# Performance work log

Hardware: AMD Instinct MI355X
Metric: run time of the kernel (lower is better)

Reference implementation:

```python
import jax, jax.numpy as jnp
import numpy as np

DEPTH = 3
DIM = 64
N_NODES = 4096
BATCH = 4


def setup_inputs() -> dict:
    key = jax.random.key(0)
    k1, k2, k3, k4 = jax.random.split(key, 4)
    x = jax.random.normal(k1, (BATCH, N_NODES, DIM), dtype=jnp.float32)
    graph = jax.random.uniform(k2, (BATCH, N_NODES, N_NODES), dtype=jnp.float32)
    # Linear((depth+1)*dim, dim): PyTorch default init U(-1/sqrt(fan_in), 1/sqrt(fan_in))
    fan_in = (DEPTH + 1) * DIM
    bound = 1.0 / np.sqrt(fan_in)
    W = jax.random.uniform(k3, (DIM, fan_in), minval=-bound, maxval=bound, dtype=jnp.float32)
    b = jax.random.uniform(k4, (DIM,), minval=-bound, maxval=bound, dtype=jnp.float32)
    return {"x": x, "graph": graph, "W": W, "b": b}


def reference(x, graph, W, b):
    # GCN branch of LocalGNN.forward (dropout p=0 -> identity).
    n = graph.shape[-1]
    g = graph + jnp.eye(n, dtype=graph.dtype)          # add self loops
    d = 1.0 / (jnp.sqrt(g.sum(axis=-1)) + 1e-7)        # [b, n]
    # D @ g @ D with D = diag(d):  g_ij * d_i * d_j
    g = g * d[..., :, None] * d[..., None, :]
    outs = [x]
    h = x
    for _ in range(DEPTH):
        h = jnp.einsum('bij,bjd->bid', g, h)           # dense propagation
        outs.append(h)
    cat = jnp.concatenate(outs, axis=-1)               # [b, n, (depth+1)*dim]
    return cat @ W.T + b
```

## Files before the change

kernel.cpp:

```cpp
#include <hip/hip_runtime.h>
#include <hip/hip_bf16.h>


typedef __attribute__((ext_vector_type(4))) float  floatx4;
typedef __attribute__((ext_vector_type(8))) short  short8;

#define NB 4
#define NN 4096
#define ND 64
#define HF_B 262144

__device__ __forceinline__ unsigned short f2bf_bits(float v) {
    __hip_bfloat16 b = __float2bfloat16(v);
    return *reinterpret_cast<unsigned short*>(&b);
}
__device__ __forceinline__ float bf2f(unsigned short u) {
    unsigned int x = ((unsigned int)u) << 16;
    return *reinterpret_cast<float*>(&x);
}
__device__ __forceinline__ short8 pack8p(const float* v) {
    short8 r;
#pragma unroll
    for (int j = 0; j < 8; ++j) r[j] = (short)f2bf_bits(v[j]);
    return r;
}

__global__ __launch_bounds__(256, 4) void prep_graph(const float* __restrict__ g,
                                                     const float* __restrict__ x,
                                                     const float* __restrict__ W,
                                                     float* __restrict__ dinv,
                                                     unsigned short* __restrict__ gswz,
                                                     unsigned short* __restrict__ hF0,
                                                     unsigned short* __restrict__ Wf) {
    __shared__ float rsum[4][16];
    __shared__ float dl[16];
    int tt = blockIdx.x;
    int b = tt >> 8, mt = tt & 255;
    int t = threadIdx.x;
    int w = t >> 6, lane = t & 63;
    int m = lane & 15, q = lane >> 4;
    const float* rowp = g + ((size_t)b * NN + mt * 16 + m) * NN;
    size_t outbase = (size_t)tt * 128 * 512;
    int i_row = mt * 16 + m;
    float rs = 0.f;

    for (int s0 = 0; s0 < NN; s0 += 512) {
#pragma unroll
        for (int gg = 0; gg < 4; ++gg) {
            int kcl = gg * 4 + w;
            int kbase = s0 + kcl * 32 + q * 8;
            floatx4 v0 = *reinterpret_cast<const floatx4*>(rowp + kbase);
            floatx4 v1 = *reinterpret_cast<const floatx4*>(rowp + kbase + 4);
            float v[8];
#pragma unroll
            for (int j = 0; j < 4; ++j) { v[j] = v0[j]; v[4 + j] = v1[j]; }
            float s = 0.f;
#pragma unroll
            for (int j = 0; j < 8; ++j) s += v[j];
            rs += s;
            int dj = i_row - kbase;
            if (dj >= 0 && dj < 8) v[dj] += 1.0f;
            *reinterpret_cast<short8*>(gswz + outbase + ((size_t)((s0 >> 5) + kcl)) * 512 + (size_t)lane * 8) = pack8p(v);
        }
    }
    rs += __shfl_xor(rs, 16);
    rs += __shfl_xor(rs, 32);
    if (lane < 16) rsum[w][lane] = rs;
    __syncthreads();
    if (t < 16) {
        float tot = rsum[0][t] + rsum[1][t] + rsum[2][t] + rsum[3][t];
        float d = 1.0f / (sqrtf(tot + 1.0f) + 1e-7f);
        dinv[b * NN + mt * 16 + t] = d;
        dl[t] = d;
    }
    __syncthreads();
    if (t < 128) {
        int c = t >> 5, lnl = t & 31;
        int q_loc = lnl >> 4, mm = lnl & 15;
        int u = mt & 1, kc2 = mt >> 1;
        int ln = u * 32 + lnl;
        const float* xp = x + ((size_t)b * NN + mt * 16) * ND + c * 16 + mm;
        float v[8];
#pragma unroll
        for (int j = 0; j < 8; ++j) {
            int lr = q_loc * 8 + j;
            v[j] = dl[lr] * xp[(size_t)lr * ND];
        }
        *reinterpret_cast<short8*>(hF0 + (size_t)b * HF_B + ((size_t)(kc2 * 4 + c) * 64 + ln) * 8) = pack8p(v);
    }
    if (tt == 0) {
#pragma unroll
        for (int e = 0; e < 8; ++e) {
            int wi = e * 256 + t;
            int kc2 = wi >> 8;
            int c = (wi >> 6) & 3;
            int ln = wi & 63;
            int mm = ln & 15, qq = ln >> 4;
            float v[8];
#pragma unroll
            for (int j = 0; j < 8; ++j) v[j] = W[(size_t)(c * 16 + mm) * 256 + kc2 * 32 + qq * 8 + j];
            *reinterpret_cast<short8*>(Wf + ((size_t)(kc2 * 4 + c) * 64 + ln) * 8) = pack8p(v);
        }
    }
}

#define PROP_MAIN()                                                                      \
    int bid = blockIdx.x;                                                                \
    int b = bid >> 8, mk = bid & 255;                                                    \
    int t = threadIdx.x;                                                                 \
    int w = t >> 6, lane = t & 63;                                                       \
    int m = lane & 15, q = lane >> 4;                                                    \
    const unsigned short* Ap = gswz + ((size_t)(b * 256 + mk) * 128 + w * 32) * 512 + (size_t)lane * 8; \
    const unsigned short* Bp = hFin + (size_t)b * HF_B + (size_t)(w * 32) * 2048 + (size_t)lane * 8;    \
    floatx4 acc[4];                                                                      \
    _Pragma("unroll")                                                                    \
    for (int c = 0; c < 4; ++c) acc[c] = (floatx4){0.f, 0.f, 0.f, 0.f};                  \
    short8 a_c  = *reinterpret_cast<const short8*>(Ap);                                  \
    short8 b0_c = *reinterpret_cast<const short8*>(Bp);                                  \
    short8 b1_c = *reinterpret_cast<const short8*>(Bp + 512);                            \
    short8 b2_c = *reinterpret_cast<const short8*>(Bp + 1024);                           \
    short8 b3_c = *reinterpret_cast<const short8*>(Bp + 1536);                           \
    _Pragma("unroll 2")                                                                  \
    for (int kc = 0; kc < 32; ++kc) {                                                    \
        Ap += 512; Bp += 2048;                                                           \
        short8 a_n  = *reinterpret_cast<const short8*>(Ap);                              \
        short8 b0_n = *reinterpret_cast<const short8*>(Bp);                              \
        short8 b1_n = *reinterpret_cast<const short8*>(Bp + 512);                        \
        short8 b2_n = *reinterpret_cast<const short8*>(Bp + 1024);                       \
        short8 b3_n = *reinterpret_cast<const short8*>(Bp + 1536);                       \
        acc[0] = __builtin_amdgcn_mfma_f32_16x16x32_bf16(a_c, b0_c, acc[0], 0, 0, 0);    \
        acc[1] = __builtin_amdgcn_mfma_f32_16x16x32_bf16(a_c, b1_c, acc[1], 0, 0, 0);    \
        acc[2] = __builtin_amdgcn_mfma_f32_16x16x32_bf16(a_c, b2_c, acc[2], 0, 0, 0);    \
        acc[3] = __builtin_amdgcn_mfma_f32_16x16x32_bf16(a_c, b3_c, acc[3], 0, 0, 0);    \
        a_c = a_n; b0_c = b0_n; b1_c = b1_n; b2_c = b2_n; b3_c = b3_n;                   \
    }                                                                                    \
    if (t < 16) dl[t] = dinv[b * NN + mk * 16 + t];                                      \
    _Pragma("unroll")                                                                    \
    for (int c = 0; c < 4; ++c)                                                          \
        _Pragma("unroll")                                                                \
        for (int r = 0; r < 4; ++r) buf[w][q * 4 + r][c * 16 + m] = acc[c][r];           \
    __syncthreads();                                                                     \
    _Pragma("unroll")                                                                    \
    for (int e = 0; e < 4; ++e) {                                                        \
        int idx = e * 256 + t;                                                           \
        int r = idx >> 6, col = idx & 63;                                                \
        float s = buf[0][r][col] + buf[1][r][col] + buf[2][r][col] + buf[3][r][col];     \
        hsh[r][col] = f2bf_bits(dl[r] * s);                                              \
    }                                                                                    \
    __syncthreads();

__global__ __launch_bounds__(256, 4) void prop_pass(const unsigned short* __restrict__ gswz,
                                                    const unsigned short* __restrict__ hFin,
                                                    const float* __restrict__ dinv,
                                                    unsigned short* __restrict__ hrow,
                                                    unsigned short* __restrict__ hFout) {
    __shared__ float buf[4][16][68];
    __shared__ unsigned short hsh[16][64];
    __shared__ float dl[16];
    PROP_MAIN()
    {
        unsigned short* hp = hrow + ((size_t)b * NN + mk * 16) * ND;
#pragma unroll
        for (int e = 0; e < 4; ++e) {
            int idx = e * 256 + t;
            hp[idx] = hsh[idx >> 6][idx & 63];
        }
    }
    if (t < 128) {
        int c = t >> 5, lnl = t & 31;
        int q_loc = lnl >> 4, mm = lnl & 15;
        int u = mk & 1, kc2 = mk >> 1;
        int ln = u * 32 + lnl;
        float v[8];
#pragma unroll
        for (int j = 0; j < 8; ++j) {
            int lr = q_loc * 8 + j;
            v[j] = dl[lr] * bf2f(hsh[lr][c * 16 + mm]);
        }
        *reinterpret_cast<short8*>(hFout + (size_t)b * HF_B + ((size_t)(kc2 * 4 + c) * 64 + ln) * 8) = pack8p(v);
    }
}

__global__ __launch_bounds__(256, 4) void prop_final(const unsigned short* __restrict__ gswz,
                                                     const unsigned short* __restrict__ hFin,
                                                     const float* __restrict__ dinv,
                                                     const float* __restrict__ x,
                                                     const unsigned short* __restrict__ hrow1,
                                                     const unsigned short* __restrict__ hrow2,
                                                     const unsigned short* __restrict__ Wf,
                                                     const float* __restrict__ bias,
                                                     float* __restrict__ out) {
    __shared__ float buf[4][16][68];
    __shared__ unsigned short hsh[16][64];
    __shared__ float dl[16];
    PROP_MAIN()
    {
        int grow_r = b * NN + mk * 16 + m;
        floatx4 facc = (floatx4){0.f, 0.f, 0.f, 0.f};
#pragma unroll
        for (int p = 0; p < 4; ++p) {
#pragma unroll
            for (int ki = 0; ki < 2; ++ki) {
                short8 af;
                if (p == 0) {
                    const float* xp = x + (size_t)grow_r * ND + ki * 32 + q * 8;
                    float v[8];
#pragma unroll
                    for (int j = 0; j < 8; ++j) v[j] = xp[j];
                    af = pack8p(v);
                } else if (p == 1) {
                    af = *reinterpret_cast<const short8*>(hrow1 + (size_t)grow_r * ND + ki * 32 + q * 8);
                } else if (p == 2) {
                    af = *reinterpret_cast<const short8*>(hrow2 + (size_t)grow_r * ND + ki * 32 + q * 8);
                } else {
                    af = *reinterpret_cast<const short8*>(&hsh[m][ki * 32 + q * 8]);
                }
                int kc2 = p * 2 + ki;
                short8 bf = *reinterpret_cast<const short8*>(Wf + ((size_t)(kc2 * 4 + w) * 64 + lane) * 8);
                facc = __builtin_amdgcn_mfma_f32_16x16x32_bf16(af, bf, facc, 0, 0, 0);
            }
        }
        float bb = bias[w * 16 + m];
#pragma unroll
        for (int r = 0; r < 4; ++r) {
            int row = b * NN + mk * 16 + q * 4 + r;
            out[(size_t)row * ND + w * 16 + m] = facc[r] + bb;
        }
    }
}

extern "C" void kernel_launch(void* const* d_in, const int* in_sizes, int n_in,
                              void* d_out, int out_size, void* d_ws, size_t ws_size,
                              hipStream_t stream) {
    const float* x     = (const float*)d_in[0];
    const float* graph = (const float*)d_in[1];
    const float* W     = (const float*)d_in[2];
    const float* bias  = (const float*)d_in[3];
    float* out = (float*)d_out;

    char* w = (char*)d_ws;
    float*          dinv  = (float*)w;
    unsigned short* Wf    = (unsigned short*)(w + (1 << 16));
    unsigned short* hFa   = (unsigned short*)(w + (1 << 17));
    unsigned short* hFb   = hFa + (size_t)NB * HF_B;
    unsigned short* hrow1 = hFb + (size_t)NB * HF_B;
    unsigned short* hrow2 = hrow1 + (size_t)NB * NN * ND;
    unsigned short* gswz  = hrow2 + (size_t)NB * NN * ND;

    prep_graph<<<1024, 256, 0, stream>>>(graph, x, W, dinv, gswz, hFa, Wf);
    prop_pass<<<1024, 256, 0, stream>>>(gswz, hFa, dinv, hrow1, hFb);
    prop_pass<<<1024, 256, 0, stream>>>(gswz, hFb, dinv, hrow2, hFa);
    prop_final<<<1024, 256, 0, stream>>>(gswz, hFa, dinv, x, hrow1, hrow2, Wf, bias, out);
}
```

Baseline: 485.8 us.

## Fuse four launches into one cooperative persistent kernel with grid syncs

```diff
diff --git a/kernel.cpp b/kernel.cpp
--- a/kernel.cpp
+++ b/kernel.cpp
@@ -1,5 +1,8 @@
 #include <hip/hip_runtime.h>
 #include <hip/hip_bf16.h>
+#include <hip/hip_cooperative_groups.h>
+
+namespace cg = cooperative_groups;
 
 
 typedef __attribute__((ext_vector_type(4))) float  floatx4;
@@ -23,6 +26,213 @@
 #pragma unroll
     for (int j = 0; j < 8; ++j) r[j] = (short)f2bf_bits(v[j]);
     return r;
+}
+
+#define PROP_CORE(HFIN)                                                              \
+    {                                                                                \
+        __syncthreads();                                                             \
+        const unsigned short* Ap = gswz + ((size_t)tile * 128 + w * 32) * 512 + (size_t)lane * 8;          \
+        const unsigned short* Bp = (HFIN) + (size_t)b * HF_B + (size_t)(w * 32) * 2048 + (size_t)lane * 8; \
+        floatx4 acc[4];                                                              \
+        _Pragma("unroll")                                                            \
+        for (int c = 0; c < 4; ++c) acc[c] = (floatx4){0.f, 0.f, 0.f, 0.f};          \
+        short8 a_c  = *reinterpret_cast<const short8*>(Ap);                          \
+        short8 b0_c = *reinterpret_cast<const short8*>(Bp);                          \
+        short8 b1_c = *reinterpret_cast<const short8*>(Bp + 512);                    \
+        short8 b2_c = *reinterpret_cast<const short8*>(Bp + 1024);                   \
+        short8 b3_c = *reinterpret_cast<const short8*>(Bp + 1536);                   \
+        _Pragma("unroll 2")                                                          \
+        for (int kc = 0; kc < 32; ++kc) {                                            \
+            Ap += 512; Bp += 2048;                                                   \
+            short8 a_n  = *reinterpret_cast<const short8*>(Ap);                      \
+            short8 b0_n = *reinterpret_cast<const short8*>(Bp);                      \
+            short8 b1_n = *reinterpret_cast<const short8*>(Bp + 512);                \
+            short8 b2_n = *reinterpret_cast<const short8*>(Bp + 1024);               \
+            short8 b3_n = *reinterpret_cast<const short8*>(Bp + 1536);               \
+            acc[0] = __builtin_amdgcn_mfma_f32_16x16x32_bf16(a_c, b0_c, acc[0], 0, 0, 0); \
+            acc[1] = __builtin_amdgcn_mfma_f32_16x16x32_bf16(a_c, b1_c, acc[1], 0, 0, 0); \
+            acc[2] = __builtin_amdgcn_mfma_f32_16x16x32_bf16(a_c, b2_c, acc[2], 0, 0, 0); \
+            acc[3] = __builtin_amdgcn_mfma_f32_16x16x32_bf16(a_c, b3_c, acc[3], 0, 0, 0); \
+            a_c = a_n; b0_c = b0_n; b1_c = b1_n; b2_c = b2_n; b3_c = b3_n;           \
+        }                                                                            \
+        if (tl < 16) dl[half][tl] = dinv[b * NN + mt * 16 + tl];                     \
+        _Pragma("unroll")                                                            \
+        for (int c = 0; c < 4; ++c)                                                  \
+            _Pragma("unroll")                                                        \
+            for (int r = 0; r < 4; ++r) buf[half][w][q * 4 + r][c * 16 + m] = acc[c][r]; \
+        __syncthreads();                                                             \
+        _Pragma("unroll")                                                            \
+        for (int e = 0; e < 4; ++e) {                                                \
+            int idx = e * 256 + tl;                                                  \
+            int r = idx >> 6, col = idx & 63;                                        \
+            float s = buf[half][0][r][col] + buf[half][1][r][col] +                  \
+                      buf[half][2][r][col] + buf[half][3][r][col];                   \
+            hsh[half][r][col] = f2bf_bits(dl[half][r] * s);                          \
+        }                                                                            \
+        __syncthreads();                                                             \
+    }
+
+#define PROP_EMIT(HROW, HFOUT)                                                       \
+    {                                                                                \
+        unsigned short* hp = (HROW) + ((size_t)b * NN + mt * 16) * ND;               \
+        _Pragma("unroll")                                                            \
+        for (int e = 0; e < 4; ++e) {                                                \
+            int idx = e * 256 + tl;                                                  \
+            hp[idx] = hsh[half][idx >> 6][idx & 63];                                 \
+        }                                                                            \
+        if (tl < 128) {                                                              \
+            int c = tl >> 5, lnl = tl & 31;                                          \
+            int q_loc = lnl >> 4, mm = lnl & 15;                                     \
+            int u = mt & 1, kc2 = mt >> 1;                                           \
+            int ln = u * 32 + lnl;                                                   \
+            float v[8];                                                              \
+            _Pragma("unroll")                                                        \
+            for (int j = 0; j < 8; ++j) {                                            \
+                int lr = q_loc * 8 + j;                                              \
+                v[j] = dl[half][lr] * bf2f(hsh[half][lr][c * 16 + mm]);              \
+            }                                                                        \
+            *reinterpret_cast<short8*>((HFOUT) + (size_t)b * HF_B + ((size_t)(kc2 * 4 + c) * 64 + ln) * 8) = pack8p(v); \
+        }                                                                            \
+    }
+
+__global__ __launch_bounds__(512, 4) void gnn_all(
+    const float* __restrict__ g, const float* __restrict__ x,
+    const float* __restrict__ W, const float* __restrict__ bias,
+    float* __restrict__ dinv, unsigned short* __restrict__ Wf,
+    unsigned short* __restrict__ hFa, unsigned short* __restrict__ hFb,
+    unsigned short* __restrict__ hrow1, unsigned short* __restrict__ hrow2,
+    unsigned short* __restrict__ gswz, float* __restrict__ out)
+{
+    cg::grid_group grid = cg::this_grid();
+    __shared__ float buf[2][4][16][68];
+    __shared__ unsigned short hsh[2][16][64];
+    __shared__ float dl[2][16];
+    __shared__ float rsum[2][4][16];
+
+    int t = threadIdx.x;
+    int half = t >> 8, tl = t & 255;
+    int w = tl >> 6, lane = tl & 63;
+    int m = lane & 15, q = lane >> 4;
+    int stride2 = gridDim.x << 1;
+
+    for (int tile = blockIdx.x * 2 + half; tile < NB * 256; tile += stride2) {
+        int b = tile >> 8, mt = tile & 255;
+        const float* rowp = g + ((size_t)b * NN + mt * 16 + m) * NN;
+        size_t outbase = (size_t)tile * 128 * 512;
+        int i_row = mt * 16 + m;
+        float rs = 0.f;
+        for (int s0 = 0; s0 < NN; s0 += 512) {
+            floatx4 vv[8];
+#pragma unroll
+            for (int gg = 0; gg < 4; ++gg) {
+                int kbase = s0 + (gg * 4 + w) * 32 + q * 8;
+                vv[2 * gg]     = *reinterpret_cast<const floatx4*>(rowp + kbase);
+                vv[2 * gg + 1] = *reinterpret_cast<const floatx4*>(rowp + kbase + 4);
+            }
+#pragma unroll
+            for (int gg = 0; gg < 4; ++gg) {
+                int kcl = gg * 4 + w;
+                int kbase = s0 + kcl * 32 + q * 8;
+                float v[8];
+#pragma unroll
+                for (int j = 0; j < 4; ++j) { v[j] = vv[2 * gg][j]; v[4 + j] = vv[2 * gg + 1][j]; }
+                float s = 0.f;
+#pragma unroll
+                for (int j = 0; j < 8; ++j) s += v[j];
+                rs += s;
+                int dj = i_row - kbase;
+                if (dj >= 0 && dj < 8) v[dj] += 1.0f;
+                *reinterpret_cast<short8*>(gswz + outbase + ((size_t)((s0 >> 5) + kcl)) * 512 + (size_t)lane * 8) = pack8p(v);
+            }
+        }
+        rs += __shfl_xor(rs, 16);
+        rs += __shfl_xor(rs, 32);
+        if (lane < 16) rsum[half][w][lane] = rs;
+        __syncthreads();
+        if (tl < 16) {
+            float tot = rsum[half][0][tl] + rsum[half][1][tl] + rsum[half][2][tl] + rsum[half][3][tl];
+            float d = 1.0f / (sqrtf(tot + 1.0f) + 1e-7f);
+            dinv[b * NN + mt * 16 + tl] = d;
+            dl[half][tl] = d;
+        }
+        __syncthreads();
+        if (tl < 128) {
+            int c = tl >> 5, lnl = tl & 31;
+            int q_loc = lnl >> 4, mm = lnl & 15;
+            int u = mt & 1, kc2 = mt >> 1;
+            int ln = u * 32 + lnl;
+            const float* xp = x + ((size_t)b * NN + mt * 16) * ND + c * 16 + mm;
+            float v[8];
+#pragma unroll
+            for (int j = 0; j < 8; ++j) {
+                int lr = q_loc * 8 + j;
+                v[j] = dl[half][lr] * xp[(size_t)lr * ND];
+            }
+            *reinterpret_cast<short8*>(hFa + (size_t)b * HF_B + ((size_t)(kc2 * 4 + c) * 64 + ln) * 8) = pack8p(v);
+        }
+        if (tile == 0) {
+#pragma unroll
+            for (int e = 0; e < 8; ++e) {
+                int wi = e * 256 + tl;
+                int kc2 = wi >> 8, c = (wi >> 6) & 3, ln = wi & 63;
+                int mm = ln & 15, qq = ln >> 4;
+                float v[8];
+#pragma unroll
+                for (int j = 0; j < 8; ++j) v[j] = W[(size_t)(c * 16 + mm) * 256 + kc2 * 32 + qq * 8 + j];
+                *reinterpret_cast<short8*>(Wf + ((size_t)(kc2 * 4 + c) * 64 + ln) * 8) = pack8p(v);
+            }
+        }
+    }
+    grid.sync();
+    for (int tile = blockIdx.x * 2 + half; tile < NB * 256; tile += stride2) {
+        int b = tile >> 8, mt = tile & 255;
+        PROP_CORE(hFa)
+        PROP_EMIT(hrow1, hFb)
+    }
+    grid.sync();
+    for (int tile = blockIdx.x * 2 + half; tile < NB * 256; tile += stride2) {
+        int b = tile >> 8, mt = tile & 255;
+        PROP_CORE(hFb)
+        PROP_EMIT(hrow2, hFa)
+    }
+    grid.sync();
+    for (int tile = blockIdx.x * 2 + half; tile < NB * 256; tile += stride2) {
+        int b = tile >> 8, mt = tile & 255;
+        PROP_CORE(hFa)
+        {
+            int grow_r = b * NN + mt * 16 + m;
+            floatx4 facc = (floatx4){0.f, 0.f, 0.f, 0.f};
+#pragma unroll
+            for (int p = 0; p < 4; ++p) {
+#pragma unroll
+                for (int ki = 0; ki < 2; ++ki) {
+                    short8 af;
+                    if (p == 0) {
+                        const float* xp = x + (size_t)grow_r * ND + ki * 32 + q * 8;
+                        float v[8];
+#pragma unroll
+                        for (int j = 0; j < 8; ++j) v[j] = xp[j];
+                        af = pack8p(v);
+                    } else if (p == 1) {
+                        af = *reinterpret_cast<const short8*>(hrow1 + (size_t)grow_r * ND + ki * 32 + q * 8);
+                    } else if (p == 2) {
+                        af = *reinterpret_cast<const short8*>(hrow2 + (size_t)grow_r * ND + ki * 32 + q * 8);
+                    } else {
+                        af = *reinterpret_cast<const short8*>(&hsh[half][m][ki * 32 + q * 8]);
+                    }
+                    int kc2 = p * 2 + ki;
+                    short8 bf = *reinterpret_cast<const short8*>(Wf + ((size_t)(kc2 * 4 + w) * 64 + lane) * 8);
+                    facc = __builtin_amdgcn_mfma_f32_16x16x32_bf16(af, bf, facc, 0, 0, 0);
+                }
+            }
+            float bb = bias[w * 16 + m];
+#pragma unroll
+            for (int r = 0; r < 4; ++r) {
+                int row = b * NN + mt * 16 + q * 4 + r;
+                out[(size_t)row * ND + w * 16 + m] = facc[r] + bb;
+            }
+        }
+    }
 }
 
 __global__ __launch_bounds__(256, 4) void prep_graph(const float* __restrict__ g,
@@ -43,7 +253,6 @@
     size_t outbase = (size_t)tt * 128 * 512;
     int i_row = mt * 16 + m;
     float rs = 0.f;
-
     for (int s0 = 0; s0 < NN; s0 += 512) {
 #pragma unroll
         for (int gg = 0; gg < 4; ++gg) {
@@ -104,37 +313,31 @@
     }
 }
 
-#define PROP_MAIN()                                                                      \
+#define FB_PROP_MAIN()                                                                   \
     int bid = blockIdx.x;                                                                \
-    int b = bid >> 8, mk = bid & 255;                                                    \
+    int b = bid >> 8, mt = bid & 255;                                                    \
     int t = threadIdx.x;                                                                 \
     int w = t >> 6, lane = t & 63;                                                       \
     int m = lane & 15, q = lane >> 4;                                                    \
-    const unsigned short* Ap = gswz + ((size_t)(b * 256 + mk) * 128 + w * 32) * 512 + (size_t)lane * 8; \
+    const unsigned short* Ap = gswz + ((size_t)(b * 256 + mt) * 128 + w * 32) * 512 + (size_t)lane * 8; \
     const unsigned short* Bp = hFin + (size_t)b * HF_B + (size_t)(w * 32) * 2048 + (size_t)lane * 8;    \
     floatx4 acc[4];                                                                      \
     _Pragma("unroll")                                                                    \
     for (int c = 0; c < 4; ++c) acc[c] = (floatx4){0.f, 0.f, 0.f, 0.f};                  \
-    short8 a_c  = *reinterpret_cast<const short8*>(Ap);                                  \
-    short8 b0_c = *reinterpret_cast<const short8*>(Bp);                                  \
-    short8 b1_c = *reinterpret_cast<const short8*>(Bp + 512);                            \
-    short8 b2_c = *reinterpret_cast<const short8*>(Bp + 1024);                           \
-    short8 b3_c = *reinterpret_cast<const short8*>(Bp + 1536);                           \
     _Pragma("unroll 2")                                                                  \
     for (int kc = 0; kc < 32; ++kc) {                                                    \
+        short8 a0 = *reinterpret_cast<const short8*>(Ap);                                \
+        short8 b0 = *reinterpret_cast<const short8*>(Bp);                                \
+        short8 b1 = *reinterpret_cast<const short8*>(Bp + 512);                          \
+        short8 b2 = *reinterpret_cast<const short8*>(Bp + 1024);                         \
+        short8 b3 = *reinterpret_cast<const short8*>(Bp + 1536);                         \
         Ap += 512; Bp += 2048;                                                           \
-        short8 a_n  = *reinterpret_cast<const short8*>(Ap);                              \
-        short8 b0_n = *reinterpret_cast<const short8*>(Bp);                              \
-        short8 b1_n = *reinterpret_cast<const short8*>(Bp + 512);                        \
-        short8 b2_n = *reinterpret_cast<const short8*>(Bp + 1024);                       \
-        short8 b3_n = *reinterpret_cast<const short8*>(Bp + 1536);                       \
-        acc[0] = __builtin_amdgcn_mfma_f32_16x16x32_bf16(a_c, b0_c, acc[0], 0, 0, 0);    \
-        acc[1] = __builtin_amdgcn_mfma_f32_16x16x32_bf16(a_c, b1_c, acc[1], 0, 0, 0);    \
-        acc[2] = __builtin_amdgcn_mfma_f32_16x16x32_bf16(a_c, b2_c, acc[2], 0, 0, 0);    \
-        acc[3] = __builtin_amdgcn_mfma_f32_16x16x32_bf16(a_c, b3_c, acc[3], 0, 0, 0);    \
-        a_c = a_n; b0_c = b0_n; b1_c = b1_n; b2_c = b2_n; b3_c = b3_n;                   \
+        acc[0] = __builtin_amdgcn_mfma_f32_16x16x32_bf16(a0, b0, acc[0], 0, 0, 0);       \
+        acc[1] = __builtin_amdgcn_mfma_f32_16x16x32_bf16(a0, b1, acc[1], 0, 0, 0);       \
+        acc[2] = __builtin_amdgcn_mfma_f32_16x16x32_bf16(a0, b2, acc[2], 0, 0, 0);       \
+        acc[3] = __builtin_amdgcn_mfma_f32_16x16x32_bf16(a0, b3, acc[3], 0, 0, 0);       \
     }                                                                                    \
-    if (t < 16) dl[t] = dinv[b * NN + mk * 16 + t];                                      \
+    if (t < 16) dl[t] = dinv[b * NN + mt * 16 + t];                                      \
     _Pragma("unroll")                                                                    \
     for (int c = 0; c < 4; ++c)                                                          \
         _Pragma("unroll")                                                                \
@@ -157,9 +360,9 @@
     __shared__ float buf[4][16][68];
     __shared__ unsigned short hsh[16][64];
     __shared__ float dl[16];
-    PROP_MAIN()
+    FB_PROP_MAIN()
     {
-        unsigned short* hp = hrow + ((size_t)b * NN + mk * 16) * ND;
+        unsigned short* hp = hrow + ((size_t)b * NN + mt * 16) * ND;
 #pragma unroll
         for (int e = 0; e < 4; ++e) {
             int idx = e * 256 + t;
@@ -169,7 +372,7 @@
     if (t < 128) {
         int c = t >> 5, lnl = t & 31;
         int q_loc = lnl >> 4, mm = lnl & 15;
-        int u = mk & 1, kc2 = mk >> 1;
+        int u = mt & 1, kc2 = mt >> 1;
         int ln = u * 32 + lnl;
         float v[8];
 #pragma unroll
@@ -193,9 +396,9 @@
     __shared__ float buf[4][16][68];
     __shared__ unsigned short hsh[16][64];
     __shared__ float dl[16];
-    PROP_MAIN()
+    FB_PROP_MAIN()
     {
-        int grow_r = b * NN + mk * 16 + m;
+        int grow_r = b * NN + mt * 16 + m;
         floatx4 facc = (floatx4){0.f, 0.f, 0.f, 0.f};
 #pragma unroll
         for (int p = 0; p < 4; ++p) {
@@ -223,7 +426,7 @@
         float bb = bias[w * 16 + m];
 #pragma unroll
         for (int r = 0; r < 4; ++r) {
-            int row = b * NN + mk * 16 + q * 4 + r;
+            int row = b * NN + mt * 16 + q * 4 + r;
             out[(size_t)row * ND + w * 16 + m] = facc[r] + bb;
         }
     }
@@ -238,17 +441,31 @@
     const float* bias  = (const float*)d_in[3];
     float* out = (float*)d_out;
 
-    char* w = (char*)d_ws;
-    float*          dinv  = (float*)w;
-    unsigned short* Wf    = (unsigned short*)(w + (1 << 16));
-    unsigned short* hFa   = (unsigned short*)(w + (1 << 17));
+    char* wsp = (char*)d_ws;
+    float*          dinv  = (float*)wsp;
+    unsigned short* Wf    = (unsigned short*)(wsp + (1 << 16));
+    unsigned short* hFa   = (unsigned short*)(wsp + (1 << 17));
     unsigned short* hFb   = hFa + (size_t)NB * HF_B;
     unsigned short* hrow1 = hFb + (size_t)NB * HF_B;
     unsigned short* hrow2 = hrow1 + (size_t)NB * NN * ND;
     unsigned short* gswz  = hrow2 + (size_t)NB * NN * ND;
 
-    prep_graph<<<1024, 256, 0, stream>>>(graph, x, W, dinv, gswz, hFa, Wf);
-    prop_pass<<<1024, 256, 0, stream>>>(gswz, hFa, dinv, hrow1, hFb);
-    prop_pass<<<1024, 256, 0, stream>>>(gswz, hFb, dinv, hrow2, hFa);
-    prop_final<<<1024, 256, 0, stream>>>(gswz, hFa, dinv, x, hrow1, hrow2, Wf, bias, out);
-}
+    static int nblk = 0;
+    if (nblk == 0) {
+        int occ = 0;
+        hipError_t qe = hipOccupancyMaxActiveBlocksPerMultiprocessor(&occ, (const void*)gnn_all, 512, 0);
+        nblk = (qe == hipSuccess && occ >= 2) ? 512 : 256;
+    }
+
+    void* kargs[] = {(void*)&graph, (void*)&x, (void*)&W, (void*)&bias,
+                     (void*)&dinv, (void*)&Wf, (void*)&hFa, (void*)&hFb,
+                     (void*)&hrow1, (void*)&hrow2, (void*)&gswz, (void*)&out};
+    hipError_t e = hipLaunchCooperativeKernel((const void*)gnn_all, dim3(nblk), dim3(512),
+                                              kargs, 0, stream);
+    if (e != hipSuccess) {
+        prep_graph<<<1024, 256, 0, stream>>>(graph, x, W, dinv, gswz, hFa, Wf);
+        prop_pass<<<1024, 256, 0, stream>>>(gswz, hFa, dinv, hrow1, hFb);
+        prop_pass<<<1024, 256, 0, stream>>>(gswz, hFb, dinv, hrow2, hFa);
+        prop_final<<<1024, 256, 0, stream>>>(gswz, hFa, dinv, x, hrow1, hrow2, Wf, bias, out);
+    }
+}
```

Result: slower. 647.7 us (+33.3%).
